# Optimization experiments

Measured on AMD Instinct MI355X. Metric: run time of the kernel, lower is better.

## Reference

```python
import jax, jax.numpy as jnp
import numpy as np

B, T, E = 65536, 50, 10


def _glorot(key, shape):
    fan_in, fan_out = shape[0], shape[-1]
    limit = np.sqrt(6.0 / (fan_in + fan_out))
    return jax.random.uniform(key, shape, jnp.float32, -limit, limit)


def setup_inputs() -> dict:
    key = jax.random.key(0)
    ks = jax.random.split(key, 20)
    inp = {
        "gru_hidden_state_inputs": jax.random.normal(ks[0], (B, T, E), jnp.float32),
        "attention_s": jax.random.uniform(ks[1], (B, T, E), jnp.float32),
        # initial hidden state: GlorotUniform(shape=(1, E)) as in the TF code
        "h0": _glorot(ks[2], (1, E)),
    }
    # R_t gate (sigmoid): input_w (with bias), hidden_w (no bias), Dense_sigmoid (with bias)
    inp["Wi_r"] = _glorot(ks[3], (E, E)); inp["bi_r"] = jnp.zeros((E,), jnp.float32)
    inp["Wh_r"] = _glorot(ks[4], (E, E))
    inp["Ws_r"] = _glorot(ks[5], (E, E)); inp["bs_r"] = jnp.zeros((E,), jnp.float32)
    # Z_t gate (sigmoid)
    inp["Wi_z"] = _glorot(ks[6], (E, E)); inp["bi_z"] = jnp.zeros((E,), jnp.float32)
    inp["Wh_z"] = _glorot(ks[7], (E, E))
    inp["Ws_z"] = _glorot(ks[8], (E, E)); inp["bs_z"] = jnp.zeros((E,), jnp.float32)
    # H_t_next candidate (tanh)
    inp["Wi_h"] = _glorot(ks[9], (E, E)); inp["bi_h"] = jnp.zeros((E,), jnp.float32)
    inp["Wh_h"] = _glorot(ks[10], (E, E))
    inp["Wt_h"] = _glorot(ks[11], (E, E)); inp["bt_h"] = jnp.zeros((E,), jnp.float32)
    return inp


def reference(gru_hidden_state_inputs, attention_s, h0,
              Wi_r, bi_r, Wh_r, Ws_r, bs_r,
              Wi_z, bi_z, Wh_z, Ws_z, bs_z,
              Wi_h, bi_h, Wh_h, Wt_h, bt_h):
    b, t, e = gru_hidden_state_inputs.shape
    h = jnp.broadcast_to(h0, (b, e))  # TF broadcasts the (1,E) init against the batch
    # scan over time: xs are [T, B, E]
    xs = (jnp.swapaxes(gru_hidden_state_inputs, 0, 1),
          jnp.swapaxes(attention_s, 0, 1))

    def step(h, xa):
        x_t, a_t = xa
        # note: each gate has an EXTRA dense layer (Dense_sigmoid / Dense_tanh are Dense layers)
        r = jax.nn.sigmoid((x_t @ Wi_r + bi_r + h @ Wh_r) @ Ws_r + bs_r)
        z = jax.nn.sigmoid((x_t @ Wi_z + bi_z + h @ Wh_z) @ Ws_z + bs_z)
        hc = jnp.tanh((x_t @ Wi_h + bi_h + (h * z) @ Wh_h) @ Wt_h + bt_h)
        Ra = a_t * r
        h_next = (1.0 - Ra) * h + Ra * hc
        return h_next, None

    h_final, _ = jax.lax.scan(step, h, xs)
    return h_final
```

## Files before the change

kernel.cpp:

```cpp
#include <hip/hip_runtime.h>

#define EDIM 10
#define TDIM 50
#define BATCH 65536
#define RPW   32
#define RPB   128


__device__ __forceinline__ float fast_sigmoid(float x) {
    float e = __expf(-x);
    return __builtin_amdgcn_rcpf(1.0f + e);
}
__device__ __forceinline__ float fast_tanh(float x) {
    float e = __expf(2.0f * x);
    return 1.0f - 2.0f * __builtin_amdgcn_rcpf(e + 1.0f);
}
__device__ __forceinline__ float lane_xchg(int pidx, float v) {
    return __int_as_float(__builtin_amdgcn_ds_bpermute(pidx, __float_as_int(v)));
}

__global__ __launch_bounds__(256, 2) void augru_main(
    const float* __restrict__ x_all, const float* __restrict__ a_all,
    const float* __restrict__ h0,
    const float* __restrict__ Wi_r, const float* __restrict__ bi_r,
    const float* __restrict__ Wh_r, const float* __restrict__ Ws_r, const float* __restrict__ bs_r,
    const float* __restrict__ Wi_z, const float* __restrict__ bi_z,
    const float* __restrict__ Wh_z, const float* __restrict__ Ws_z, const float* __restrict__ bs_z,
    const float* __restrict__ Wi_h, const float* __restrict__ bi_h,
    const float* __restrict__ Wh_h, const float* __restrict__ Wt_h, const float* __restrict__ bt_h,
    float* __restrict__ out)
{
    __shared__ __align__(16) float WA[480];
    __shared__ __align__(16) float WB[480];
    __shared__ __align__(16) float WBI[48];

    for (int s = threadIdx.x; s < 630; s += 256) {
        int g, kind, k, e;
        if (s < 30)       { kind = 0; g = s / 10;            k = 0;               e = s % 10; }
        else if (s < 330) { kind = 1; int q = s - 30;  g = q / 100; k = (q % 100) / 10; e = q % 10; }
        else              { kind = 2; int q = s - 330; g = q / 100; k = (q % 100) / 10; e = q % 10; }
        const float* Wi = (g == 0) ? Wi_r : (g == 1) ? Wi_z : Wi_h;
        const float* Wh = (g == 0) ? Wh_r : (g == 1) ? Wh_z : Wh_h;
        const float* Ws = (g == 0) ? Ws_r : (g == 1) ? Ws_z : Wt_h;
        const float* bi = (g == 0) ? bi_r : (g == 1) ? bi_z : bi_h;
        const float* bs = (g == 0) ? bs_r : (g == 1) ? bs_z : bt_h;
        float v = 0.0f;
        if (kind == 0) {
            v = bs[e];
            #pragma unroll
            for (int j2 = 0; j2 < 10; j2++) v += bi[j2] * Ws[j2 * 10 + e];
        } else {
            const float* M = (kind == 1) ? Wi : Wh;
            #pragma unroll
            for (int j2 = 0; j2 < 10; j2++) v += M[k * 10 + j2] * Ws[j2 * 10 + e];
        }
        int hh = e / 5, j = e % 5;
        if (kind == 0)      WBI[(g * 2 + hh) * 8 + j] = v;
        else if (kind == 1) WA[((g * 10 + k) * 2 + hh) * 8 + j] = v;
        else                WB[((g * 10 + k) * 2 + hh) * 8 + j] = v;
    }
    __syncthreads();

    const int lane = threadIdx.x & 63;
    const int wv   = threadIdx.x >> 6;
    const int half = lane >> 5;
    const int rl   = lane & 31;
    const int row  = blockIdx.x * RPB + wv * RPW + rl;
    const int pidx = (lane ^ 32) << 2;

    float wbO[3][5][5], wbP[3][5][5];
    #pragma unroll
    for (int g = 0; g < 3; g++)
        #pragma unroll
        for (int k5 = 0; k5 < 5; k5++)
            #pragma unroll
            for (int j = 0; j < 5; j++) {
                wbO[g][k5][j] = WB[((g * 10 + half * 5 + k5) * 2 + half) * 8 + j];
                wbP[g][k5][j] = WB[((g * 10 + (1 - half) * 5 + k5) * 2 + half) * 8 + j];
            }

    const float2* xp2 = (const float2*)(x_all + (size_t)row * (TDIM * EDIM));
    const float*  arp = a_all + (size_t)row * (TDIM * EDIM) + half * 5;
    float* orow = out + (size_t)row * EDIM + half * 5;

    float h[5], ph[5];
    #pragma unroll
    for (int j = 0; j < 5; j++) h[j]  = h0[half * 5 + j];
    #pragma unroll
    for (int j = 0; j < 5; j++) ph[j] = h0[(1 - half) * 5 + j];

    float2 xc[5]; float ac[5];
    #pragma unroll
    for (int i = 0; i < 5; i++) xc[i] = xp2[i];
    #pragma unroll
    for (int j = 0; j < 5; j++) ac[j] = arp[j];

    int wofs = 0;

    #pragma unroll 1
    for (int t = 0; t < TDIM; t++) {
        asm volatile("" : "+v"(wofs));
        const float* wa  = (const float*)WA  + half * 8 + wofs;
        const float* wbi = (const float*)WBI + half * 8 + wofs;

        int tn = (t < TDIM - 1) ? (t + 1) : t;
        float2 xn[5]; float an[5];
        #pragma unroll
        for (int i = 0; i < 5; i++) xn[i] = xp2[tn * 5 + i];
        #pragma unroll
        for (int j = 0; j < 5; j++) an[j] = arp[tn * 10 + j];

        float ur[5], uz[5];
        {
            float4 b4r = *(const float4*)(wbi + 0);
            float4 b4z = *(const float4*)(wbi + 16);
            ur[0] = b4r.x; ur[1] = b4r.y; ur[2] = b4r.z; ur[3] = b4r.w; ur[4] = wbi[4];
            uz[0] = b4z.x; uz[1] = b4z.y; uz[2] = b4z.z; uz[3] = b4z.w; uz[4] = wbi[20];
        }
        #pragma unroll
        for (int k = 0; k < 10; k++) {
            float xk = (k & 1) ? xc[k >> 1].y : xc[k >> 1].x;
            float4 w4 = *(const float4*)(wa + k * 16);
            float  w1 = wa[k * 16 + 4];
            ur[0] = fmaf(xk, w4.x, ur[0]); ur[1] = fmaf(xk, w4.y, ur[1]);
            ur[2] = fmaf(xk, w4.z, ur[2]); ur[3] = fmaf(xk, w4.w, ur[3]);
            ur[4] = fmaf(xk, w1,   ur[4]);
        }
        #pragma unroll
        for (int k = 0; k < 10; k++) {
            float xk = (k & 1) ? xc[k >> 1].y : xc[k >> 1].x;
            float4 w4 = *(const float4*)(wa + 160 + k * 16);
            float  w1 = wa[160 + k * 16 + 4];
            uz[0] = fmaf(xk, w4.x, uz[0]); uz[1] = fmaf(xk, w4.y, uz[1]);
            uz[2] = fmaf(xk, w4.z, uz[2]); uz[3] = fmaf(xk, w4.w, uz[3]);
            uz[4] = fmaf(xk, w1,   uz[4]);
        }
        #pragma unroll
        for (int k5 = 0; k5 < 5; k5++)
            #pragma unroll
            for (int j = 0; j < 5; j++) {
                ur[j] = fmaf(h[k5], wbO[0][k5][j], ur[j]);
                uz[j] = fmaf(h[k5], wbO[1][k5][j], uz[j]);
            }
        #pragma unroll
        for (int k5 = 0; k5 < 5; k5++)
            #pragma unroll
            for (int j = 0; j < 5; j++) {
                ur[j] = fmaf(ph[k5], wbP[0][k5][j], ur[j]);
                uz[j] = fmaf(ph[k5], wbP[1][k5][j], uz[j]);
            }

        float z5[5], hzo[5], phz[5];
        #pragma unroll
        for (int j = 0; j < 5; j++) { z5[j] = fast_sigmoid(uz[j]); hzo[j] = h[j] * z5[j]; }
        #pragma unroll
        for (int j = 0; j < 5; j++) phz[j] = lane_xchg(pidx, hzo[j]);

        float uh[5];
        {
            float4 b4h = *(const float4*)(wbi + 32);
            uh[0] = b4h.x; uh[1] = b4h.y; uh[2] = b4h.z; uh[3] = b4h.w; uh[4] = wbi[36];
        }
        #pragma unroll
        for (int k = 0; k < 10; k++) {
            float xk = (k & 1) ? xc[k >> 1].y : xc[k >> 1].x;
            float4 w4 = *(const float4*)(wa + 320 + k * 16);
            float  w1 = wa[320 + k * 16 + 4];
            uh[0] = fmaf(xk, w4.x, uh[0]); uh[1] = fmaf(xk, w4.y, uh[1]);
            uh[2] = fmaf(xk, w4.z, uh[2]); uh[3] = fmaf(xk, w4.w, uh[3]);
            uh[4] = fmaf(xk, w1,   uh[4]);
        }
        #pragma unroll
        for (int k5 = 0; k5 < 5; k5++)
            #pragma unroll
            for (int j = 0; j < 5; j++) uh[j] = fmaf(hzo[k5], wbO[2][k5][j], uh[j]);
        #pragma unroll
        for (int k5 = 0; k5 < 5; k5++)
            #pragma unroll
            for (int j = 0; j < 5; j++) uh[j] = fmaf(phz[k5], wbP[2][k5][j], uh[j]);

        #pragma unroll
        for (int j = 0; j < 5; j++) {
            float r  = fast_sigmoid(ur[j]);
            float hc = fast_tanh(uh[j]);
            float Ra = ac[j] * r;
            h[j] = fmaf(Ra, hc - h[j], h[j]);
        }

        #pragma unroll
        for (int j = 0; j < 5; j++) ph[j] = lane_xchg(pidx, h[j]);

        #pragma unroll
        for (int i = 0; i < 5; i++) xc[i] = xn[i];
        #pragma unroll
        for (int j = 0; j < 5; j++) ac[j] = an[j];
    }

    #pragma unroll
    for (int j = 0; j < 5; j++) orow[j] = h[j];
}

extern "C" void kernel_launch(void* const* d_in, const int* in_sizes, int n_in,
                              void* d_out, int out_size, void* d_ws, size_t ws_size,
                              hipStream_t stream) {
    augru_main<<<BATCH / RPB, 256, 0, stream>>>(
        (const float*)d_in[0],  (const float*)d_in[1],  (const float*)d_in[2],
        (const float*)d_in[3],  (const float*)d_in[4],  (const float*)d_in[5],
        (const float*)d_in[6],  (const float*)d_in[7],
        (const float*)d_in[8],  (const float*)d_in[9],  (const float*)d_in[10],
        (const float*)d_in[11], (const float*)d_in[12],
        (const float*)d_in[13], (const float*)d_in[14], (const float*)d_in[15],
        (const float*)d_in[16], (const float*)d_in[17],
        (float*)d_out);
}
```

Baseline: 343.0 us.

## Use one thread per row with scalar-loaded collapsed weights from constant memory

Moves the weight collapse into a separate single-block prep kernel that writes the folded matrices to a global device array. The main kernel now assigns one full row per thread instead of splitting each row across two half-waves, so the ds_bpermute exchanges and per-lane LDS weight reads go away. Weights are read through the constant address space with a wave-uniform offset, so they can be fetched with scalar loads. The costs are an extra kernel launch, half as many threads overall, more registers per thread, and wider strided per-thread reads of x and a.

New measurement: 353.8 us. +3.1%, slower.

```diff
diff --git a/kernel.cpp b/kernel.cpp
--- a/kernel.cpp
+++ b/kernel.cpp
@@ -3,9 +3,11 @@
 #define EDIM 10
 #define TDIM 50
 #define BATCH 65536
-#define RPW   32
-#define RPB   128
+#define CWN 640
 
+__device__ float g_cw[CWN];
+
+typedef const __attribute__((address_space(4))) float cfloat;
 
 __device__ __forceinline__ float fast_sigmoid(float x) {
     float e = __expf(-x);
@@ -15,28 +17,18 @@
     float e = __expf(2.0f * x);
     return 1.0f - 2.0f * __builtin_amdgcn_rcpf(e + 1.0f);
 }
-__device__ __forceinline__ float lane_xchg(int pidx, float v) {
-    return __int_as_float(__builtin_amdgcn_ds_bpermute(pidx, __float_as_int(v)));
-}
 
-__global__ __launch_bounds__(256, 2) void augru_main(
-    const float* __restrict__ x_all, const float* __restrict__ a_all,
-    const float* __restrict__ h0,
+__global__ void collapse_weights(
     const float* __restrict__ Wi_r, const float* __restrict__ bi_r,
     const float* __restrict__ Wh_r, const float* __restrict__ Ws_r, const float* __restrict__ bs_r,
     const float* __restrict__ Wi_z, const float* __restrict__ bi_z,
     const float* __restrict__ Wh_z, const float* __restrict__ Ws_z, const float* __restrict__ bs_z,
     const float* __restrict__ Wi_h, const float* __restrict__ bi_h,
-    const float* __restrict__ Wh_h, const float* __restrict__ Wt_h, const float* __restrict__ bt_h,
-    float* __restrict__ out)
+    const float* __restrict__ Wh_h, const float* __restrict__ Wt_h, const float* __restrict__ bt_h)
 {
-    __shared__ __align__(16) float WA[480];
-    __shared__ __align__(16) float WB[480];
-    __shared__ __align__(16) float WBI[48];
-
     for (int s = threadIdx.x; s < 630; s += 256) {
         int g, kind, k, e;
-        if (s < 30)       { kind = 0; g = s / 10;            k = 0;               e = s % 10; }
+        if (s < 30)       { kind = 0; g = s / 10;      k = 0;                e = s % 10; }
         else if (s < 330) { kind = 1; int q = s - 30;  g = q / 100; k = (q % 100) / 10; e = q % 10; }
         else              { kind = 2; int q = s - 330; g = q / 100; k = (q % 100) / 10; e = q % 10; }
         const float* Wi = (g == 0) ? Wi_r : (g == 1) ? Wi_z : Wi_h;
@@ -48,139 +40,104 @@
         if (kind == 0) {
             v = bs[e];
             #pragma unroll
-            for (int j2 = 0; j2 < 10; j2++) v += bi[j2] * Ws[j2 * 10 + e];
+            for (int j = 0; j < 10; j++) v += bi[j] * Ws[j * 10 + e];
         } else {
             const float* M = (kind == 1) ? Wi : Wh;
             #pragma unroll
-            for (int j2 = 0; j2 < 10; j2++) v += M[k * 10 + j2] * Ws[j2 * 10 + e];
+            for (int j = 0; j < 10; j++) v += M[k * 10 + j] * Ws[j * 10 + e];
         }
-        int hh = e / 5, j = e % 5;
-        if (kind == 0)      WBI[(g * 2 + hh) * 8 + j] = v;
-        else if (kind == 1) WA[((g * 10 + k) * 2 + hh) * 8 + j] = v;
-        else                WB[((g * 10 + k) * 2 + hh) * 8 + j] = v;
+        g_cw[s] = v;
     }
-    __syncthreads();
+}
 
-    const int lane = threadIdx.x & 63;
-    const int wv   = threadIdx.x >> 6;
-    const int half = lane >> 5;
-    const int rl   = lane & 31;
-    const int row  = blockIdx.x * RPB + wv * RPW + rl;
-    const int pidx = (lane ^ 32) << 2;
+__global__ __launch_bounds__(256, 1) void augru_main(
+    const float* __restrict__ x_all, const float* __restrict__ a_all,
+    const float* __restrict__ h0,
+    float* __restrict__ out)
+{
+    const int row = blockIdx.x * 256 + threadIdx.x;
 
-    float wbO[3][5][5], wbP[3][5][5];
+    cfloat* cw = (cfloat*)(uintptr_t)(const float*)g_cw;
+
+    const float2* xp = (const float2*)(x_all + (size_t)row * (TDIM * EDIM));
+    const float2* ap = (const float2*)(a_all + (size_t)row * (TDIM * EDIM));
+
+    float h[10];
     #pragma unroll
-    for (int g = 0; g < 3; g++)
-        #pragma unroll
-        for (int k5 = 0; k5 < 5; k5++)
-            #pragma unroll
-            for (int j = 0; j < 5; j++) {
-                wbO[g][k5][j] = WB[((g * 10 + half * 5 + k5) * 2 + half) * 8 + j];
-                wbP[g][k5][j] = WB[((g * 10 + (1 - half) * 5 + k5) * 2 + half) * 8 + j];
-            }
+    for (int j = 0; j < 10; j++) h[j] = h0[j];
 
-    const float2* xp2 = (const float2*)(x_all + (size_t)row * (TDIM * EDIM));
-    const float*  arp = a_all + (size_t)row * (TDIM * EDIM) + half * 5;
-    float* orow = out + (size_t)row * EDIM + half * 5;
+    float xc[10], ac[10];
+    #pragma unroll
+    for (int i = 0; i < 5; i++) {
+        float2 v = xp[i]; xc[2 * i] = v.x; xc[2 * i + 1] = v.y;
+        float2 u = ap[i]; ac[2 * i] = u.x; ac[2 * i + 1] = u.y;
+    }
 
-    float h[5], ph[5];
-    #pragma unroll
-    for (int j = 0; j < 5; j++) h[j]  = h0[half * 5 + j];
-    #pragma unroll
-    for (int j = 0; j < 5; j++) ph[j] = h0[(1 - half) * 5 + j];
-
-    float2 xc[5]; float ac[5];
-    #pragma unroll
-    for (int i = 0; i < 5; i++) xc[i] = xp2[i];
-    #pragma unroll
-    for (int j = 0; j < 5; j++) ac[j] = arp[j];
-
-    int wofs = 0;
+    int sofs = 0;
 
     #pragma unroll 1
     for (int t = 0; t < TDIM; t++) {
-        asm volatile("" : "+v"(wofs));
-        const float* wa  = (const float*)WA  + half * 8 + wofs;
-        const float* wbi = (const float*)WBI + half * 8 + wofs;
+        asm volatile("" : "+s"(sofs));
+        cfloat* w = cw + sofs;
 
         int tn = (t < TDIM - 1) ? (t + 1) : t;
-        float2 xn[5]; float an[5];
+        float xn[10], an[10];
         #pragma unroll
-        for (int i = 0; i < 5; i++) xn[i] = xp2[tn * 5 + i];
+        for (int i = 0; i < 5; i++) {
+            float2 v = xp[tn * 5 + i]; xn[2 * i] = v.x; xn[2 * i + 1] = v.y;
+            float2 u = ap[tn * 5 + i]; an[2 * i] = u.x; an[2 * i + 1] = u.y;
+        }
+
+        float ur[10], uz[10], uh[10];
         #pragma unroll
-        for (int j = 0; j < 5; j++) an[j] = arp[tn * 10 + j];
+        for (int j = 0; j < 10; j++) {
+            ur[j] = w[j]; uz[j] = w[10 + j]; uh[j] = w[20 + j];
+        }
 
-        float ur[5], uz[5];
-        {
-            float4 b4r = *(const float4*)(wbi + 0);
-            float4 b4z = *(const float4*)(wbi + 16);
-            ur[0] = b4r.x; ur[1] = b4r.y; ur[2] = b4r.z; ur[3] = b4r.w; ur[4] = wbi[4];
-            uz[0] = b4z.x; uz[1] = b4z.y; uz[2] = b4z.z; uz[3] = b4z.w; uz[4] = wbi[20];
+        #pragma unroll
+        for (int k = 0; k < 10; k++) {
+            float xk = xc[k];
+            #pragma unroll
+            for (int j = 0; j < 10; j++) ur[j] = fmaf(xk, w[30 + k * 10 + j], ur[j]);
         }
         #pragma unroll
         for (int k = 0; k < 10; k++) {
-            float xk = (k & 1) ? xc[k >> 1].y : xc[k >> 1].x;
-            float4 w4 = *(const float4*)(wa + k * 16);
-            float  w1 = wa[k * 16 + 4];
-            ur[0] = fmaf(xk, w4.x, ur[0]); ur[1] = fmaf(xk, w4.y, ur[1]);
-            ur[2] = fmaf(xk, w4.z, ur[2]); ur[3] = fmaf(xk, w4.w, ur[3]);
-            ur[4] = fmaf(xk, w1,   ur[4]);
+            float xk = xc[k];
+            #pragma unroll
+            for (int j = 0; j < 10; j++) uz[j] = fmaf(xk, w[130 + k * 10 + j], uz[j]);
         }
         #pragma unroll
         for (int k = 0; k < 10; k++) {
-            float xk = (k & 1) ? xc[k >> 1].y : xc[k >> 1].x;
-            float4 w4 = *(const float4*)(wa + 160 + k * 16);
-            float  w1 = wa[160 + k * 16 + 4];
-            uz[0] = fmaf(xk, w4.x, uz[0]); uz[1] = fmaf(xk, w4.y, uz[1]);
-            uz[2] = fmaf(xk, w4.z, uz[2]); uz[3] = fmaf(xk, w4.w, uz[3]);
-            uz[4] = fmaf(xk, w1,   uz[4]);
-        }
-        #pragma unroll
-        for (int k5 = 0; k5 < 5; k5++)
+            float hk = h[k];
             #pragma unroll
-            for (int j = 0; j < 5; j++) {
-                ur[j] = fmaf(h[k5], wbO[0][k5][j], ur[j]);
-                uz[j] = fmaf(h[k5], wbO[1][k5][j], uz[j]);
-            }
-        #pragma unroll
-        for (int k5 = 0; k5 < 5; k5++)
-            #pragma unroll
-            for (int j = 0; j < 5; j++) {
-                ur[j] = fmaf(ph[k5], wbP[0][k5][j], ur[j]);
-                uz[j] = fmaf(ph[k5], wbP[1][k5][j], uz[j]);
-            }
-
-        float z5[5], hzo[5], phz[5];
-        #pragma unroll
-        for (int j = 0; j < 5; j++) { z5[j] = fast_sigmoid(uz[j]); hzo[j] = h[j] * z5[j]; }
-        #pragma unroll
-        for (int j = 0; j < 5; j++) phz[j] = lane_xchg(pidx, hzo[j]);
-
-        float uh[5];
-        {
-            float4 b4h = *(const float4*)(wbi + 32);
-            uh[0] = b4h.x; uh[1] = b4h.y; uh[2] = b4h.z; uh[3] = b4h.w; uh[4] = wbi[36];
+            for (int j = 0; j < 10; j++) ur[j] = fmaf(hk, w[330 + k * 10 + j], ur[j]);
         }
         #pragma unroll
         for (int k = 0; k < 10; k++) {
-            float xk = (k & 1) ? xc[k >> 1].y : xc[k >> 1].x;
-            float4 w4 = *(const float4*)(wa + 320 + k * 16);
-            float  w1 = wa[320 + k * 16 + 4];
-            uh[0] = fmaf(xk, w4.x, uh[0]); uh[1] = fmaf(xk, w4.y, uh[1]);
-            uh[2] = fmaf(xk, w4.z, uh[2]); uh[3] = fmaf(xk, w4.w, uh[3]);
-            uh[4] = fmaf(xk, w1,   uh[4]);
+            float hk = h[k];
+            #pragma unroll
+            for (int j = 0; j < 10; j++) uz[j] = fmaf(hk, w[430 + k * 10 + j], uz[j]);
         }
         #pragma unroll
-        for (int k5 = 0; k5 < 5; k5++)
+        for (int k = 0; k < 10; k++) {
+            float xk = xc[k];
             #pragma unroll
-            for (int j = 0; j < 5; j++) uh[j] = fmaf(hzo[k5], wbO[2][k5][j], uh[j]);
+            for (int j = 0; j < 10; j++) uh[j] = fmaf(xk, w[230 + k * 10 + j], uh[j]);
+        }
+
+        float hz[10];
         #pragma unroll
-        for (int k5 = 0; k5 < 5; k5++)
-            #pragma unroll
-            for (int j = 0; j < 5; j++) uh[j] = fmaf(phz[k5], wbP[2][k5][j], uh[j]);
+        for (int j = 0; j < 10; j++) hz[j] = h[j] * fast_sigmoid(uz[j]);
 
         #pragma unroll
-        for (int j = 0; j < 5; j++) {
+        for (int k = 0; k < 10; k++) {
+            float hk = hz[k];
+            #pragma unroll
+            for (int j = 0; j < 10; j++) uh[j] = fmaf(hk, w[530 + k * 10 + j], uh[j]);
+        }
+
+        #pragma unroll
+        for (int j = 0; j < 10; j++) {
             float r  = fast_sigmoid(ur[j]);
             float hc = fast_tanh(uh[j]);
             float Ra = ac[j] * r;
@@ -188,28 +145,25 @@
         }
 
         #pragma unroll
-        for (int j = 0; j < 5; j++) ph[j] = lane_xchg(pidx, h[j]);
-
-        #pragma unroll
-        for (int i = 0; i < 5; i++) xc[i] = xn[i];
-        #pragma unroll
-        for (int j = 0; j < 5; j++) ac[j] = an[j];
+        for (int j = 0; j < 10; j++) { xc[j] = xn[j]; ac[j] = an[j]; }
     }
 
+    float2* orow = (float2*)(out + (size_t)row * EDIM);
     #pragma unroll
-    for (int j = 0; j < 5; j++) orow[j] = h[j];
+    for (int i = 0; i < 5; i++) orow[i] = make_float2(h[2 * i], h[2 * i + 1]);
 }
 
 extern "C" void kernel_launch(void* const* d_in, const int* in_sizes, int n_in,
                               void* d_out, int out_size, void* d_ws, size_t ws_size,
                               hipStream_t stream) {
-    augru_main<<<BATCH / RPB, 256, 0, stream>>>(
-        (const float*)d_in[0],  (const float*)d_in[1],  (const float*)d_in[2],
+    collapse_weights<<<1, 256, 0, stream>>>(
         (const float*)d_in[3],  (const float*)d_in[4],  (const float*)d_in[5],
         (const float*)d_in[6],  (const float*)d_in[7],
         (const float*)d_in[8],  (const float*)d_in[9],  (const float*)d_in[10],
         (const float*)d_in[11], (const float*)d_in[12],
         (const float*)d_in[13], (const float*)d_in[14], (const float*)d_in[15],
-        (const float*)d_in[16], (const float*)d_in[17],
+        (const float*)d_in[16], (const float*)d_in[17]);
+    augru_main<<<BATCH / 256, 256, 0, stream>>>(
+        (const float*)d_in[0], (const float*)d_in[1], (const float*)d_in[2],
         (float*)d_out);
 }
```
